# Kernel optimization log

Measured on AMD Instinct MI355X. Metric: run time of the kernel, lower is better.

The kernel has to match this reference:

```python
import jax, jax.numpy as jnp
import numpy as np

C = 256
EPS = 1e-5

def layer_norm(x, g, b):
    mu = jnp.mean(x, axis=-1, keepdims=True)
    var = jnp.var(x, axis=-1, keepdims=True)
    return (x - mu) * jax.lax.rsqrt(var + EPS) * g + b

def setup_inputs() -> dict:
    key = jax.random.key(0)
    ks = jax.random.split(key, 12)
    B, H, W = 1, 64, 64
    s = 1.0 / np.sqrt(C)
    inp = {
        'lidar_features': jax.random.normal(ks[0], (B, C, H, W), jnp.float32),
        'image_features': jax.random.normal(ks[1], (B, C, H, W), jnp.float32),
        'Wq': jax.random.normal(ks[2], (C, C), jnp.float32) * s,
        'bq': jnp.zeros((C,), jnp.float32),
        'Wk': jax.random.normal(ks[3], (C, C), jnp.float32) * s,
        'bk': jnp.zeros((C,), jnp.float32),
        'Wv': jax.random.normal(ks[4], (C, C), jnp.float32) * s,
        'bv': jnp.zeros((C,), jnp.float32),
        'Wo': jax.random.normal(ks[5], (C, C), jnp.float32) * s,
        'bo': jnp.zeros((C,), jnp.float32),
        'g1': jnp.ones((C,), jnp.float32),
        'b1': jnp.zeros((C,), jnp.float32),
        'W1': jax.random.normal(ks[6], (C, 4 * C), jnp.float32) * s,
        'bf1': jnp.zeros((4 * C,), jnp.float32),
        'W2': jax.random.normal(ks[7], (4 * C, C), jnp.float32) * (1.0 / np.sqrt(4 * C)),
        'bf2': jnp.zeros((C,), jnp.float32),
        'g2': jnp.ones((C,), jnp.float32),
        'b2': jnp.zeros((C,), jnp.float32),
        'num_heads': 8,
    }
    return inp

def reference(lidar_features, image_features, Wq, bq, Wk, bk, Wv, bv, Wo, bo,
              g1, b1, W1, bf1, W2, bf2, g2, b2, num_heads):
    B, Cc, H, W = lidar_features.shape
    S = H * W
    hd = Cc // num_heads
    # [B,C,H,W] -> [B,S,C]
    x = lidar_features.reshape(B, Cc, S).transpose(0, 2, 1)
    y = image_features.reshape(B, Cc, S).transpose(0, 2, 1)
    q = x @ Wq + bq            # [B,S,C]
    k = y @ Wk + bk
    v = y @ Wv + bv
    qh = q.reshape(B, S, num_heads, hd).transpose(0, 2, 1, 3)  # [B,h,S,d]
    kh = k.reshape(B, S, num_heads, hd).transpose(0, 2, 1, 3)
    vh = v.reshape(B, S, num_heads, hd).transpose(0, 2, 1, 3)
    attn = jnp.einsum('bhqd,bhkd->bhqk', qh, kh) / jnp.sqrt(jnp.float32(hd))
    attn = jax.nn.softmax(attn, axis=-1)
    out = jnp.einsum('bhqk,bhkd->bhqd', attn, vh)
    out = out.transpose(0, 2, 1, 3).reshape(B, S, Cc)
    out = out @ Wo + bo
    # residual is the projected q in [B,S,C] layout (intended semantics)
    out = layer_norm(q + out, g1, b1)
    ffn = jax.nn.relu(out @ W1 + bf1) @ W2 + bf2
    out = layer_norm(out + ffn, g2, b2)
    return out.reshape(B, H, W, Cc).transpose(0, 3, 1, 2)
```

## Files before the change

kernel.cpp:

```cpp
#include <hip/hip_runtime.h>

#define SQ 4096
#define CCH 256
#define NH 8
#define HD 32
#define LN_EPS 1e-5f
#define NSPLIT 4
#define VROWS 48

typedef __bf16 bf16x8 __attribute__((ext_vector_type(8)));
typedef float f32x4 __attribute__((ext_vector_type(4)));
using bf16 = __bf16;

__device__ __forceinline__ float fast_exp2(float x) {
#if defined(__has_builtin)
#if __has_builtin(__builtin_amdgcn_exp2f)
    return __builtin_amdgcn_exp2f(x);
#else
    float r;
    asm("v_exp_f32 %0, %1" : "=v"(r) : "v"(x));
    return r;
#endif
#else
    float r;
    asm("v_exp_f32 %0, %1" : "=v"(r) : "v"(x));
    return r;
#endif
}

__device__ __forceinline__ void tile_tc(const float* __restrict__ src, bf16* __restrict__ dst,
                                        int R, int Ccol, int ti, int tj) {
    __shared__ float t[32][33];
    const int tx = threadIdx.x & 31;
    const int ty = threadIdx.x >> 5;
    const int i0 = ti * 32, j0 = tj * 32;
    #pragma unroll
    for (int i = 0; i < 32; i += 8)
        t[ty + i][tx] = src[(size_t)(i0 + ty + i) * Ccol + j0 + tx];
    __syncthreads();
    #pragma unroll
    for (int i = 0; i < 32; i += 8)
        dst[(size_t)(j0 + ty + i) * R + i0 + tx] = (bf16)t[tx][ty + i];
}

__global__ __launch_bounds__(256)
void cvt_inputs(const float* __restrict__ x, const float* __restrict__ y,
                bf16* __restrict__ xT, bf16* __restrict__ yT) {
    const float* s = blockIdx.z ? y : x;
    bf16* d = blockIdx.z ? yT : xT;
    tile_tc(s, d, CCH, SQ, blockIdx.y, blockIdx.x);
}

__global__ __launch_bounds__(256)
void cvt_weights(const float* Wq, const float* Wk, const float* Wv, const float* Wo,
                 const float* W1, const float* W2,
                 bf16* WqT, bf16* WkT, bf16* WvT, bf16* WoT, bf16* W1T, bf16* W2T,
                 bf16* vTb) {
    const int id = blockIdx.x;
    if (id < 256) {
        const int w = id >> 6, local = id & 63;
        const float* s = (w == 0) ? Wq : (w == 1) ? Wk : (w == 2) ? Wv : Wo;
        bf16* d = (w == 0) ? WqT : (w == 1) ? WkT : (w == 2) ? WvT : WoT;
        tile_tc(s, d, 256, 256, local >> 3, local & 7);
    } else if (id < 512) {
        const int local = id - 256;
        tile_tc(W1, W1T, 256, 1024, local >> 5, local & 31);
    } else if (id < 768) {
        const int local = id - 512;
        tile_tc(W2, W2T, 1024, 256, local >> 3, local & 7);
    } else {
        const int local = id - 768;
        #pragma unroll
        for (int rr = 0; rr < 2; ++rr) {
            const int pr = local * 2 + rr;
            const int hh = pr >> 4, j = pr & 15;
            const bf16 val = (bf16)((j == 0) ? 1.0f : 0.0f);
            bf16x8 v8;
            #pragma unroll
            for (int e = 0; e < 8; ++e) v8[e] = val;
            bf16* dst = vTb + ((size_t)hh * VROWS + 32 + j) * SQ + threadIdx.x * 16;
            *reinterpret_cast<bf16x8*>(dst) = v8;
            *reinterpret_cast<bf16x8*>(dst + 8) = v8;
        }
    }
}

template <int K, int OUT_MODE, bool RELU>
__global__ __launch_bounds__(256)
void gemm_mfma(const bf16* __restrict__ A, const bf16* __restrict__ BT,
               const float* __restrict__ bias, float* __restrict__ Cf,
               bf16* __restrict__ Cb, int N) {
    const int tid = threadIdx.x;
    const int w = tid >> 6, l = tid & 63;
    const int l15 = l & 15, lg = l >> 4;
    const int m0 = blockIdx.x * 64 + (w >> 1) * 32;
    const int n0 = blockIdx.y * 64 + (w & 1) * 32;

    f32x4 acc[2][2] = {};
    const bf16* a0 = &A[(size_t)(m0 + l15) * K + lg * 8];
    const bf16* b0 = &BT[(size_t)(n0 + l15) * K + lg * 8];

    for (int k0 = 0; k0 < K; k0 += 32) {
        bf16x8 a[2], b[2];
        a[0] = *reinterpret_cast<const bf16x8*>(a0 + k0);
        a[1] = *reinterpret_cast<const bf16x8*>(a0 + (size_t)16 * K + k0);
        b[0] = *reinterpret_cast<const bf16x8*>(b0 + k0);
        b[1] = *reinterpret_cast<const bf16x8*>(b0 + (size_t)16 * K + k0);
        #pragma unroll
        for (int i = 0; i < 2; ++i)
            #pragma unroll
            for (int j = 0; j < 2; ++j)
                acc[i][j] = __builtin_amdgcn_mfma_f32_16x16x32_bf16(a[i], b[j], acc[i][j], 0, 0, 0);
    }

    #pragma unroll
    for (int i = 0; i < 2; ++i) {
        #pragma unroll
        for (int j = 0; j < 2; ++j) {
            const int col = n0 + j * 16 + l15;
            const float bs = bias[col];
            #pragma unroll
            for (int r = 0; r < 4; ++r) {
                const int row = m0 + i * 16 + lg * 4 + r;
                float val = acc[i][j][r] + bs;
                if (RELU) val = fmaxf(val, 0.f);
                if constexpr (OUT_MODE == 0)
                    Cf[(size_t)row * N + col] = val;
                if constexpr (OUT_MODE == 2)
                    Cb[(size_t)row * N + col] = (bf16)val;
            }
        }
    }
}

template <int K, int KS>
__global__ __launch_bounds__(256)
void gemm_sk(const bf16* __restrict__ A, const bf16* __restrict__ BT,
             const float* __restrict__ bias, float* __restrict__ Cf, int N) {
    constexpr int KSL = K / KS;
    const int z = blockIdx.z;
    const int tid = threadIdx.x;
    const int w = tid >> 6, l = tid & 63;
    const int l15 = l & 15, lg = l >> 4;
    const int m0 = blockIdx.x * 64 + (w >> 1) * 32;
    const int n0 = blockIdx.y * 64 + (w & 1) * 32;

    f32x4 acc[2][2] = {};
    const bf16* a0 = &A[(size_t)(m0 + l15) * K + z * KSL + lg * 8];
    const bf16* b0 = &BT[(size_t)(n0 + l15) * K + z * KSL + lg * 8];

    for (int k0 = 0; k0 < KSL; k0 += 32) {
        bf16x8 a[2], b[2];
        a[0] = *reinterpret_cast<const bf16x8*>(a0 + k0);
        a[1] = *reinterpret_cast<const bf16x8*>(a0 + (size_t)16 * K + k0);
        b[0] = *reinterpret_cast<const bf16x8*>(b0 + k0);
        b[1] = *reinterpret_cast<const bf16x8*>(b0 + (size_t)16 * K + k0);
        #pragma unroll
        for (int i = 0; i < 2; ++i)
            #pragma unroll
            for (int j = 0; j < 2; ++j)
                acc[i][j] = __builtin_amdgcn_mfma_f32_16x16x32_bf16(a[i], b[j], acc[i][j], 0, 0, 0);
    }

    float* C = Cf + (size_t)z * SQ * N;
    #pragma unroll
    for (int i = 0; i < 2; ++i) {
        #pragma unroll
        for (int j = 0; j < 2; ++j) {
            const int col = n0 + j * 16 + l15;
            const float bs = (z == 0) ? bias[col] : 0.f;
            #pragma unroll
            for (int r = 0; r < 4; ++r) {
                const int row = m0 + i * 16 + lg * 4 + r;
                C[(size_t)row * N + col] = acc[i][j][r] + bs;
            }
        }
    }
}

__global__ __launch_bounds__(256)
void qkv_gemm(const bf16* __restrict__ xT, const bf16* __restrict__ yT,
              const bf16* __restrict__ WqT, const bf16* __restrict__ WkT,
              const bf16* __restrict__ WvT,
              const float* __restrict__ bq, const float* __restrict__ bk,
              const float* __restrict__ bv,
              bf16* __restrict__ qb, bf16* __restrict__ kbb, bf16* __restrict__ vTb,
              float kscale) {
    const int z = blockIdx.z;
    const bf16* A  = (z == 0) ? xT : yT;
    const bf16* BT = (z == 0) ? WqT : (z == 1) ? WkT : WvT;
    const float* bias = (z == 0) ? bq : (z == 1) ? bk : bv;

    const int tid = threadIdx.x;
    const int w = tid >> 6, l = tid & 63;
    const int l15 = l & 15, lg = l >> 4;
    const int m0 = blockIdx.x * 64 + (w >> 1) * 32;
    const int n0 = blockIdx.y * 64 + (w & 1) * 32;

    f32x4 acc[2][2] = {};
    const bf16* a0 = &A[(size_t)(m0 + l15) * CCH + lg * 8];
    const bf16* b0 = &BT[(size_t)(n0 + l15) * CCH + lg * 8];

    for (int k0 = 0; k0 < CCH; k0 += 32) {
        bf16x8 a[2], b[2];
        a[0] = *reinterpret_cast<const bf16x8*>(a0 + k0);
        a[1] = *reinterpret_cast<const bf16x8*>(a0 + (size_t)16 * CCH + k0);
        b[0] = *reinterpret_cast<const bf16x8*>(b0 + k0);
        b[1] = *reinterpret_cast<const bf16x8*>(b0 + (size_t)16 * CCH + k0);
        #pragma unroll
        for (int i = 0; i < 2; ++i)
            #pragma unroll
            for (int j = 0; j < 2; ++j)
                acc[i][j] = __builtin_amdgcn_mfma_f32_16x16x32_bf16(a[i], b[j], acc[i][j], 0, 0, 0);
    }

    const float sc = (z == 1) ? kscale : 1.f;
    #pragma unroll
    for (int i = 0; i < 2; ++i) {
        #pragma unroll
        for (int j = 0; j < 2; ++j) {
            const int col = n0 + j * 16 + l15;
            const float bs = bias[col];
            #pragma unroll
            for (int r = 0; r < 4; ++r) {
                const int row = m0 + i * 16 + lg * 4 + r;
                float val = acc[i][j][r] + bs;
                if (z == 2)
                    vTb[((size_t)(col >> 5) * VROWS + (col & 31)) * SQ + row] = (bf16)val;
                else if (z == 1)
                    kbb[(size_t)row * CCH + col] = (bf16)(val * sc);
                else
                    qb[(size_t)row * CCH + col] = (bf16)val;
            }
        }
    }
}

__global__ __launch_bounds__(256)
void flash_attn11(const bf16* __restrict__ qb, const bf16* __restrict__ kb,
                  const bf16* __restrict__ vT, bf16* __restrict__ Op,
                  float* __restrict__ Lp) {
    const int fid = blockIdx.x + 16 * (blockIdx.y + NH * blockIdx.z);
    const int nid = (fid & 7) * 64 + (fid >> 3);
    const int q0 = (nid & 15) * 256;
    const int h  = (nid >> 4) & 7;
    const int sp = nid >> 7;

    const int tid = threadIdx.x;
    const int w = tid >> 6, l = tid & 63;
    const int l15 = l & 15, lg = l >> 4;

    __shared__ unsigned int Sb[4][2][8][72];

    bf16x8 aq[4];
    #pragma unroll
    for (int su = 0; su < 4; ++su)
        aq[su] = *reinterpret_cast<const bf16x8*>(
            &qb[(size_t)(q0 + su * 64 + w * 16 + l15) * CCH + h * HD + lg * 8]);

    f32x4 o[4][2] = {};
    f32x4 o2[4] = {};

    const bf16* kfrag = &kb[(size_t)l15 * CCH + h * HD + lg * 8];
    const bf16* vfrag = &vT[((size_t)h * VROWS + l15) * SQ + lg * 8];

    const int kt0 = sp * (SQ / NSPLIT / 64);
    const int kt1 = kt0 + (SQ / NSPLIT / 64);

    for (int kt = kt0; kt < kt1; ++kt) {
        const int kb0 = kt * 64;

        bf16x8 kf[4], vf[3][2];
        #pragma unroll
        for (int t = 0; t < 4; ++t)
            kf[t] = *reinterpret_cast<const bf16x8*>(kfrag + (size_t)(kb0 + t * 16) * CCH);
        #pragma unroll
        for (int dh = 0; dh < 3; ++dh)
            #pragma unroll
            for (int kh = 0; kh < 2; ++kh)
                vf[dh][kh] = *reinterpret_cast<const bf16x8*>(
                    vfrag + (size_t)dh * 16 * SQ + kb0 + kh * 32);

        #pragma unroll
        for (int su = 0; su < 4; ++su) {
            const int par = su & 1;
            f32x4 s[4];
            #pragma unroll
            for (int t = 0; t < 4; ++t)
                s[t] = __builtin_amdgcn_mfma_f32_16x16x32_bf16(
                    kf[t], aq[su], (f32x4){0.f, 0.f, 0.f, 0.f}, 0, 0, 0);

            #pragma unroll
            for (int t = 0; t < 4; ++t) {
                unsigned int u0 = __builtin_bit_cast(unsigned int, fast_exp2(s[t][0]));
                unsigned int u1 = __builtin_bit_cast(unsigned int, fast_exp2(s[t][1]));
                unsigned int u2 = __builtin_bit_cast(unsigned int, fast_exp2(s[t][2]));
                unsigned int u3 = __builtin_bit_cast(unsigned int, fast_exp2(s[t][3]));
                Sb[w][par][t * 2 + 0][l] = __builtin_amdgcn_perm(u1, u0, 0x07060302u);
                Sb[w][par][t * 2 + 1][l] = __builtin_amdgcn_perm(u3, u2, 0x07060302u);
            }

            #pragma unroll
            for (int kh = 0; kh < 2; ++kh) {
                const int sbase = kh * 4 + (lg >> 1) * 2;
                const int i0 = l15 + 16 * ((lg & 1) * 2);
                const int i1 = i0 + 16;
                union { unsigned int u[4]; bf16x8 v; } pb;
                pb.u[0] = Sb[w][par][sbase + 0][i0];
                pb.u[1] = Sb[w][par][sbase + 1][i0];
                pb.u[2] = Sb[w][par][sbase + 0][i1];
                pb.u[3] = Sb[w][par][sbase + 1][i1];
                #pragma unroll
                for (int dh = 0; dh < 2; ++dh)
                    o[su][dh] = __builtin_amdgcn_mfma_f32_16x16x32_bf16(
                        vf[dh][kh], pb.v, o[su][dh], 0, 0, 0);
                o2[su] = __builtin_amdgcn_mfma_f32_16x16x32_bf16(
                    vf[2][kh], pb.v, o2[su], 0, 0, 0);
            }
        }
    }

    const size_t obase = ((size_t)sp * NH + h) * HD;
    #pragma unroll
    for (int su = 0; su < 4; ++su) {
        const int qrow = q0 + su * 64 + w * 16 + l15;
        #pragma unroll
        for (int dh = 0; dh < 2; ++dh)
            #pragma unroll
            for (int r = 0; r < 4; ++r)
                Op[(obase + dh * 16 + lg * 4 + r) * SQ + qrow] = (bf16)o[su][dh][r];
        if (lg == 0)
            Lp[((size_t)sp * NH + h) * SQ + qrow] = o2[su][0];
    }
}

__global__ __launch_bounds__(256)
void attn_merge3(const bf16* __restrict__ Op, const float* __restrict__ Lp,
                 bf16* __restrict__ atb) {
    const int h = blockIdx.y;
    const int q0 = blockIdx.x * 64;
    const int t = threadIdx.x;
    __shared__ float sInv[64];
    __shared__ float trans[32][65];

    if (t < 64) {
        float L = 0.f;
        #pragma unroll
        for (int sp = 0; sp < NSPLIT; ++sp)
            L += Lp[((size_t)sp * NH + h) * SQ + q0 + t];
        sInv[t] = 1.0f / L;
    }
    __syncthreads();

    const int q = t & 63, dg = t >> 6;
    float a[8] = {0.f, 0.f, 0.f, 0.f, 0.f, 0.f, 0.f, 0.f};
    for (int sp = 0; sp < NSPLIT; ++sp) {
        const size_t rb = ((size_t)sp * NH + h) * HD;
        #pragma unroll
        for (int i = 0; i < 8; ++i) {
            const int d = i * 4 + dg;
            a[i] += (float)Op[(rb + d) * SQ + q0 + q];
        }
    }
    const float invq = sInv[q];
    #pragma unroll
    for (int i = 0; i < 8; ++i)
        trans[i * 4 + dg][q] = a[i] * invq;
    __syncthreads();

    const int oq = t >> 2, od = (t & 3) * 8;
    bf16x8 o8;
    #pragma unroll
    for (int j = 0; j < 8; ++j) o8[j] = (bf16)trans[od + j][oq];
    *reinterpret_cast<bf16x8*>(&atb[(size_t)(q0 + oq) * CCH + h * HD + od]) = o8;
}

__global__ __launch_bounds__(256)
void add_ln1(const bf16* __restrict__ a, const float* __restrict__ b,
             const float* __restrict__ g, const float* __restrict__ beta,
             float* __restrict__ out, bf16* __restrict__ outb) {
    const int s = blockIdx.x;
    const int c = threadIdx.x;
    const size_t idx = (size_t)s * CCH + c;
    float val = (float)a[idx] + b[idx] + b[idx + (size_t)SQ * CCH];
    float sum = val, sq = val * val;
    #pragma unroll
    for (int off = 1; off < 64; off <<= 1) {
        sum += __shfl_xor(sum, off);
        sq  += __shfl_xor(sq, off);
    }
    __shared__ float ssum[4], ssq[4];
    int w = c >> 6;
    if ((c & 63) == 0) { ssum[w] = sum; ssq[w] = sq; }
    __syncthreads();
    sum = ssum[0] + ssum[1] + ssum[2] + ssum[3];
    sq  = ssq[0] + ssq[1] + ssq[2] + ssq[3];
    float mu = sum * (1.0f / CCH);
    float var = sq * (1.0f / CCH) - mu * mu;
    float rs = rsqrtf(var + LN_EPS);
    float res = (val - mu) * rs * g[c] + beta[c];
    out[idx] = res;
    outb[idx] = (bf16)res;
}

__global__ __launch_bounds__(256)
void add_ln_t(const float* __restrict__ a, const float* __restrict__ b,
              const float* __restrict__ g, const float* __restrict__ beta,
              float* __restrict__ out) {
    const int s0 = blockIdx.x * 32;
    const int t = threadIdx.x;
    const int row = t >> 3;
    const int e8 = t & 7;
    const size_t base = (size_t)(s0 + row) * CCH + e8 * 32;
    const size_t PS = (size_t)SQ * CCH;

    float v[32];
    float sum = 0.f, sq = 0.f;
    #pragma unroll
    for (int j = 0; j < 32; j += 4) {
        float4 va = *reinterpret_cast<const float4*>(&a[base + j]);
        float4 vb = *reinterpret_cast<const float4*>(&b[base + j]);
        float4 vc = *reinterpret_cast<const float4*>(&b[base + PS + j]);
        v[j]     = va.x + vb.x + vc.x;
        v[j + 1] = va.y + vb.y + vc.y;
        v[j + 2] = va.z + vb.z + vc.z;
        v[j + 3] = va.w + vb.w + vc.w;
        sum += (v[j] + v[j + 1]) + (v[j + 2] + v[j + 3]);
        sq  += (v[j] * v[j] + v[j + 1] * v[j + 1]) + (v[j + 2] * v[j + 2] + v[j + 3] * v[j + 3]);
    }
    sum += __shfl_xor(sum, 1); sum += __shfl_xor(sum, 2); sum += __shfl_xor(sum, 4);
    sq  += __shfl_xor(sq, 1);  sq  += __shfl_xor(sq, 2);  sq  += __shfl_xor(sq, 4);
    const float mu = sum * (1.0f / CCH);
    const float var = sq * (1.0f / CCH) - mu * mu;
    const float rs = rsqrtf(var + LN_EPS);
    #pragma unroll
    for (int j = 0; j < 32; j += 4) {
        float4 gg = *reinterpret_cast<const float4*>(&g[e8 * 32 + j]);
        float4 bb = *reinterpret_cast<const float4*>(&beta[e8 * 32 + j]);
        v[j]     = (v[j]     - mu) * rs * gg.x + bb.x;
        v[j + 1] = (v[j + 1] - mu) * rs * gg.y + bb.y;
        v[j + 2] = (v[j + 2] - mu) * rs * gg.z + bb.z;
        v[j + 3] = (v[j + 3] - mu) * rs * gg.w + bb.w;
    }

    __shared__ float tile[32][33];
    const int cl = t >> 3, f4 = (t & 7) * 4;
    for (int c = 0; c < 8; ++c) {
        __syncthreads();
        if (e8 == c) {
            #pragma unroll
            for (int j = 0; j < 32; ++j) tile[j][row] = v[j];
        }
        __syncthreads();
        float4 o4 = {tile[cl][f4], tile[cl][f4 + 1], tile[cl][f4 + 2], tile[cl][f4 + 3]};
        *reinterpret_cast<float4*>(&out[(size_t)(c * 32 + cl) * SQ + s0 + f4]) = o4;
    }
}

extern "C" void kernel_launch(void* const* d_in, const int* in_sizes, int n_in,
                              void* d_out, int out_size, void* d_ws, size_t ws_size,
                              hipStream_t stream) {
    const float* lidar = (const float*)d_in[0];
    const float* image = (const float*)d_in[1];
    const float* Wq  = (const float*)d_in[2];
    const float* bq  = (const float*)d_in[3];
    const float* Wk  = (const float*)d_in[4];
    const float* bk  = (const float*)d_in[5];
    const float* Wv  = (const float*)d_in[6];
    const float* bv  = (const float*)d_in[7];
    const float* Wo  = (const float*)d_in[8];
    const float* bo  = (const float*)d_in[9];
    const float* g1  = (const float*)d_in[10];
    const float* b1  = (const float*)d_in[11];
    const float* W1  = (const float*)d_in[12];
    const float* bf1 = (const float*)d_in[13];
    const float* W2  = (const float*)d_in[14];
    const float* bf2 = (const float*)d_in[15];
    const float* g2  = (const float*)d_in[16];
    const float* b2  = (const float*)d_in[17];
    float* out = (float*)d_out;

    char* ws = (char*)d_ws;
    const size_t KB = 1024;
    bf16* W2T = (bf16*)(ws + 0);
    bf16* W1T = (bf16*)(ws + 512 * KB);
    bf16* WoT = (bf16*)(ws + 1024 * KB);
    bf16* WqT = (bf16*)(ws + 1152 * KB);
    bf16* WkT = (bf16*)(ws + 1280 * KB);
    bf16* WvT = (bf16*)(ws + 1408 * KB);
    bf16* qb  = (bf16*)(ws + 1536 * KB);
    bf16* kbb = (bf16*)(ws + 3584 * KB);
    bf16* vTb = (bf16*)(ws + 5632 * KB);
    bf16* xT  = (bf16*)(ws + 8704 * KB);
    bf16* yT  = (bf16*)(ws + 10752 * KB);
    bf16* Op  = (bf16*)(ws + 8704 * KB);
    float* Lp = (float*)d_out;
    bf16* atb = (bf16*)(ws + 3584 * KB);
    float* o01 = (float*)(ws + 8704 * KB);
    float* ln1 = (float*)(ws + 19968 * KB);
    bf16* ln1b = (bf16*)(ws + 5632 * KB);
    bf16* h1  = (bf16*)(ws + 9728 * KB);
    float* h2 = (float*)(ws + 1536 * KB);

    const float qscale = 0.17677669529663687f * 1.4426950408889634f;
    dim3 blk(256);

    cvt_inputs<<<dim3(SQ / 32, CCH / 32, 2), blk, 0, stream>>>(lidar, image, xT, yT);
    cvt_weights<<<dim3(832), blk, 0, stream>>>(Wq, Wk, Wv, Wo, W1, W2,
                                               WqT, WkT, WvT, WoT, W1T, W2T, vTb);
    qkv_gemm<<<dim3(64, 4, 3), blk, 0, stream>>>(xT, yT, WqT, WkT, WvT,
                                                 bq, bk, bv, qb, kbb, vTb, qscale);
    flash_attn11<<<dim3(SQ / 256, NH, NSPLIT), blk, 0, stream>>>(qb, kbb, vTb, Op, Lp);
    attn_merge3<<<dim3(SQ / 64, NH), blk, 0, stream>>>(Op, Lp, atb);
    gemm_sk<256, 2><<<dim3(64, 4, 2), blk, 0, stream>>>(atb, WoT, bo, o01, 256);
    add_ln1<<<SQ, blk, 0, stream>>>(qb, o01, g1, b1, ln1, ln1b);
    gemm_mfma<256, 2, true><<<dim3(64, 16), blk, 0, stream>>>(ln1b, W1T, bf1, nullptr, h1, 1024);
    gemm_sk<1024, 2><<<dim3(64, 4, 2), blk, 0, stream>>>(h1, W2T, bf2, h2, 256);
    add_ln_t<<<dim3(SQ / 32), blk, 0, stream>>>(ln1, h2, g2, b2, out);
}
```

Measured before the change: 137.7 us.

## Fuse Wo projection with residual LayerNorm and merge conversion kernels

Replaces the split-K Wo GEMM plus separate add+LayerNorm kernel with a single kernel. Each block computes 16 full rows of the projection with MFMA, adds bias and the q residual, and reduces mean and variance across the four waves through shared memory. This removes the fp32 partial-sum round trip through global memory and one launch. The input and weight conversion kernels are also merged into one launch. In exchange, the fused GEMM uses small 16-row tiles that reload the Wo weights per block and give less reuse.

```diff
diff --git a/kernel.cpp b/kernel.cpp
--- a/kernel.cpp
+++ b/kernel.cpp
@@ -44,32 +44,35 @@
 }
 
 __global__ __launch_bounds__(256)
-void cvt_inputs(const float* __restrict__ x, const float* __restrict__ y,
-                bf16* __restrict__ xT, bf16* __restrict__ yT) {
-    const float* s = blockIdx.z ? y : x;
-    bf16* d = blockIdx.z ? yT : xT;
-    tile_tc(s, d, CCH, SQ, blockIdx.y, blockIdx.x);
-}
-
-__global__ __launch_bounds__(256)
-void cvt_weights(const float* Wq, const float* Wk, const float* Wv, const float* Wo,
-                 const float* W1, const float* W2,
-                 bf16* WqT, bf16* WkT, bf16* WvT, bf16* WoT, bf16* W1T, bf16* W2T,
-                 bf16* vTb) {
+void cvt_all(const float* __restrict__ x, const float* __restrict__ y,
+             bf16* __restrict__ xT, bf16* __restrict__ yT,
+             const float* Wq, const float* Wk, const float* Wv, const float* Wo,
+             const float* W1, const float* W2,
+             bf16* WqT, bf16* WkT, bf16* WvT, bf16* WoT, bf16* W1T, bf16* W2T,
+             bf16* vTb) {
     const int id = blockIdx.x;
-    if (id < 256) {
-        const int w = id >> 6, local = id & 63;
+    if (id < 2048) {
+        const int z = id >> 10;
+        const int t = id & 1023;
+        const float* s = z ? y : x;
+        bf16* d = z ? yT : xT;
+        tile_tc(s, d, CCH, SQ, t >> 7, t & 127);
+        return;
+    }
+    const int wid = id - 2048;
+    if (wid < 256) {
+        const int w = wid >> 6, local = wid & 63;
         const float* s = (w == 0) ? Wq : (w == 1) ? Wk : (w == 2) ? Wv : Wo;
         bf16* d = (w == 0) ? WqT : (w == 1) ? WkT : (w == 2) ? WvT : WoT;
         tile_tc(s, d, 256, 256, local >> 3, local & 7);
-    } else if (id < 512) {
-        const int local = id - 256;
+    } else if (wid < 512) {
+        const int local = wid - 256;
         tile_tc(W1, W1T, 256, 1024, local >> 5, local & 31);
-    } else if (id < 768) {
-        const int local = id - 512;
+    } else if (wid < 768) {
+        const int local = wid - 512;
         tile_tc(W2, W2T, 1024, 256, local >> 3, local & 7);
     } else {
-        const int local = id - 768;
+        const int local = wid - 768;
         #pragma unroll
         for (int rr = 0; rr < 2; ++rr) {
             const int pr = local * 2 + rr;
@@ -232,6 +235,87 @@
                 else
                     qb[(size_t)row * CCH + col] = (bf16)val;
             }
+        }
+    }
+}
+
+__global__ __launch_bounds__(256)
+void wo_ln1(const bf16* __restrict__ atb, const bf16* __restrict__ WoT,
+            const float* __restrict__ bo, const bf16* __restrict__ qb,
+            const float* __restrict__ g, const float* __restrict__ beta,
+            float* __restrict__ ln1, bf16* __restrict__ ln1b) {
+    const int tid = threadIdx.x;
+    const int w = tid >> 6, l = tid & 63;
+    const int l15 = l & 15, lg = l >> 4;
+    const int mr = blockIdx.x * 16;
+    const int n0 = w * 64;
+
+    f32x4 acc[4] = {};
+    const bf16* a0 = &atb[(size_t)(mr + l15) * CCH + lg * 8];
+    const bf16* b0 = &WoT[(size_t)(n0 + l15) * CCH + lg * 8];
+    #pragma unroll
+    for (int k0 = 0; k0 < CCH; k0 += 32) {
+        bf16x8 a = *reinterpret_cast<const bf16x8*>(a0 + k0);
+        #pragma unroll
+        for (int j = 0; j < 4; ++j) {
+            bf16x8 b = *reinterpret_cast<const bf16x8*>(b0 + (size_t)j * 16 * CCH + k0);
+            acc[j] = __builtin_amdgcn_mfma_f32_16x16x32_bf16(a, b, acc[j], 0, 0, 0);
+        }
+    }
+
+    float val[4][4];
+    float rsum[4] = {0.f, 0.f, 0.f, 0.f}, rsq[4] = {0.f, 0.f, 0.f, 0.f};
+    #pragma unroll
+    for (int j = 0; j < 4; ++j) {
+        const int col = n0 + j * 16 + l15;
+        const float bs = bo[col];
+        #pragma unroll
+        for (int r = 0; r < 4; ++r) {
+            const int row = mr + lg * 4 + r;
+            float v = acc[j][r] + bs + (float)qb[(size_t)row * CCH + col];
+            val[j][r] = v;
+            rsum[r] += v;
+            rsq[r] += v * v;
+        }
+    }
+    #pragma unroll
+    for (int r = 0; r < 4; ++r) {
+        #pragma unroll
+        for (int off = 1; off < 16; off <<= 1) {
+            rsum[r] += __shfl_xor(rsum[r], off);
+            rsq[r]  += __shfl_xor(rsq[r], off);
+        }
+    }
+    __shared__ float ssum[4][16], ssq[4][16];
+    if (l15 == 0) {
+        #pragma unroll
+        for (int r = 0; r < 4; ++r) {
+            ssum[w][lg * 4 + r] = rsum[r];
+            ssq[w][lg * 4 + r]  = rsq[r];
+        }
+    }
+    __syncthreads();
+    float mu_[4], rs_[4];
+    #pragma unroll
+    for (int r = 0; r < 4; ++r) {
+        const int row = lg * 4 + r;
+        float s = (ssum[0][row] + ssum[1][row]) + (ssum[2][row] + ssum[3][row]);
+        float q = (ssq[0][row] + ssq[1][row]) + (ssq[2][row] + ssq[3][row]);
+        float mu = s * (1.0f / CCH);
+        float var = q * (1.0f / CCH) - mu * mu;
+        mu_[r] = mu;
+        rs_[r] = rsqrtf(var + LN_EPS);
+    }
+    #pragma unroll
+    for (int j = 0; j < 4; ++j) {
+        const int col = n0 + j * 16 + l15;
+        const float gg = g[col], bb = beta[col];
+        #pragma unroll
+        for (int r = 0; r < 4; ++r) {
+            const int row = mr + lg * 4 + r;
+            float res = (val[j][r] - mu_[r]) * rs_[r] * gg + bb;
+            ln1[(size_t)row * CCH + col] = res;
+            ln1b[(size_t)row * CCH + col] = (bf16)res;
         }
     }
 }
@@ -373,34 +457,6 @@
     #pragma unroll
     for (int j = 0; j < 8; ++j) o8[j] = (bf16)trans[od + j][oq];
     *reinterpret_cast<bf16x8*>(&atb[(size_t)(q0 + oq) * CCH + h * HD + od]) = o8;
-}
-
-__global__ __launch_bounds__(256)
-void add_ln1(const bf16* __restrict__ a, const float* __restrict__ b,
-             const float* __restrict__ g, const float* __restrict__ beta,
-             float* __restrict__ out, bf16* __restrict__ outb) {
-    const int s = blockIdx.x;
-    const int c = threadIdx.x;
-    const size_t idx = (size_t)s * CCH + c;
-    float val = (float)a[idx] + b[idx] + b[idx + (size_t)SQ * CCH];
-    float sum = val, sq = val * val;
-    #pragma unroll
-    for (int off = 1; off < 64; off <<= 1) {
-        sum += __shfl_xor(sum, off);
-        sq  += __shfl_xor(sq, off);
-    }
-    __shared__ float ssum[4], ssq[4];
-    int w = c >> 6;
-    if ((c & 63) == 0) { ssum[w] = sum; ssq[w] = sq; }
-    __syncthreads();
-    sum = ssum[0] + ssum[1] + ssum[2] + ssum[3];
-    sq  = ssq[0] + ssq[1] + ssq[2] + ssq[3];
-    float mu = sum * (1.0f / CCH);
-    float var = sq * (1.0f / CCH) - mu * mu;
-    float rs = rsqrtf(var + LN_EPS);
-    float res = (val - mu) * rs * g[c] + beta[c];
-    out[idx] = res;
-    outb[idx] = (bf16)res;
 }
 
 __global__ __launch_bounds__(256)
@@ -496,7 +552,6 @@
     bf16* Op  = (bf16*)(ws + 8704 * KB);
     float* Lp = (float*)d_out;
     bf16* atb = (bf16*)(ws + 3584 * KB);
-    float* o01 = (float*)(ws + 8704 * KB);
     float* ln1 = (float*)(ws + 19968 * KB);
     bf16* ln1b = (bf16*)(ws + 5632 * KB);
     bf16* h1  = (bf16*)(ws + 9728 * KB);
@@ -505,15 +560,14 @@
     const float qscale = 0.17677669529663687f * 1.4426950408889634f;
     dim3 blk(256);
 
-    cvt_inputs<<<dim3(SQ / 32, CCH / 32, 2), blk, 0, stream>>>(lidar, image, xT, yT);
-    cvt_weights<<<dim3(832), blk, 0, stream>>>(Wq, Wk, Wv, Wo, W1, W2,
-                                               WqT, WkT, WvT, WoT, W1T, W2T, vTb);
+    cvt_all<<<dim3(2880), blk, 0, stream>>>(lidar, image, xT, yT,
+                                            Wq, Wk, Wv, Wo, W1, W2,
+                                            WqT, WkT, WvT, WoT, W1T, W2T, vTb);
     qkv_gemm<<<dim3(64, 4, 3), blk, 0, stream>>>(xT, yT, WqT, WkT, WvT,
                                                  bq, bk, bv, qb, kbb, vTb, qscale);
     flash_attn11<<<dim3(SQ / 256, NH, NSPLIT), blk, 0, stream>>>(qb, kbb, vTb, Op, Lp);
     attn_merge3<<<dim3(SQ / 64, NH), blk, 0, stream>>>(Op, Lp, atb);
-    gemm_sk<256, 2><<<dim3(64, 4, 2), blk, 0, stream>>>(atb, WoT, bo, o01, 256);
-    add_ln1<<<SQ, blk, 0, stream>>>(qb, o01, g1, b1, ln1, ln1b);
+    wo_ln1<<<dim3(SQ / 16), blk, 0, stream>>>(atb, WoT, bo, qb, g1, b1, ln1, ln1b);
     gemm_mfma<256, 2, true><<<dim3(64, 16), blk, 0, stream>>>(ln1b, W1T, bf1, nullptr, h1, 1024);
     gemm_sk<1024, 2><<<dim3(64, 4, 2), blk, 0, stream>>>(h1, W2T, bf2, h2, 256);
     add_ln_t<<<dim3(SQ / 32), blk, 0, stream>>>(ln1, h2, g2, b2, out);
```

After: 128.7 us. 6.6% less time.
